# Kernel tuning notes

Measured on AMD Instinct MI355X. Metric: run time of the kernel, lower is better.

## Reference

```python
import jax, jax.numpy as jnp
import numpy as np
import math

B, HQ, HK, M, N, D, S, O, SO = 4, 32, 8, 16, 8192, 128, 256, 8, 64


def _make_proj_score(key):
    # __init__: randn proj, then per-D-column-chunk QR (rot=True), scaled by sqrt(D)
    proj = jax.random.normal(key, (D, S), dtype=jnp.float32)
    chunks = []
    for i in range(0, S, D):
        q, _ = jnp.linalg.qr(proj[:, i:i + D])
        chunks.append(q)
    return (jnp.concatenate(chunks, axis=-1) * math.sqrt(D)).astype(jnp.float32)


def setup_inputs() -> dict:
    key = jax.random.key(0)
    k1, k2, k3, k4 = jax.random.split(key, 4)
    return {
        "query": jax.random.normal(k1, (B, HQ, M, D), dtype=jnp.float32),
        "data": jax.random.normal(k2, (B, HK, N, D), dtype=jnp.float32),
        "proj_dir_score": _make_proj_score(k3),
        "outlier_indices": jax.random.randint(k4, (B, HK, N, O), 0, D, dtype=jnp.int32),
        "dim_outlier": SO,
    }


def reference(query, data, proj_dir_score, outlier_indices, dim_outlier):
    # query: [B,Hq,M,D] fp32; data (keys): [B,Hk,N,D]; proj_dir_score: [D,S]
    Bb, Hk, Nn, Dd = data.shape
    Hq, Mq = query.shape[1], query.shape[2]
    G = Hq // Hk  # GQA repeat factor (repeat_interleave along heads)
    Ss = proj_dir_score.shape[1]
    So = dim_outlier
    dt = data.dtype

    # --- qjl_quant: split keys into inlier / outlier channels per key ---
    # scatter a 0/1 outlier-channel mask: [B,Hk,N,D]
    flat_idx = outlier_indices.reshape(-1, outlier_indices.shape[-1])
    rows = jnp.arange(flat_idx.shape[0])[:, None]
    mask = jnp.zeros((flat_idx.shape[0], Dd), dt).at[rows, flat_idx].set(1.0)
    mask = mask.reshape(Bb, Hk, Nn, Dd)

    k_out = data * mask          # outlier channels only
    k_in = data - k_out          # outlier channels zeroed
    norm_in = jnp.linalg.norm(k_in, axis=-1)    # [B,Hk,N]
    norm_out = jnp.linalg.norm(k_out, axis=-1)  # [B,Hk,N]

    # 1-bit sign-JL quantization (bit-packed in the CUDA kernel; +-1 floats here)
    sign_in = jnp.sign(jnp.einsum('bhnd,ds->bhns', k_in, proj_dir_score))   # [B,Hk,N,S]
    proj_out = proj_dir_score[:, :So]                                       # [D,So]
    sign_out = jnp.sign(jnp.einsum('bhnd,ds->bhns', k_out, proj_out))       # [B,Hk,N,So]

    # --- qjl_gqa_score: QJL unbiased inner-product estimator ---
    # <q,k> ~= sqrt(pi/2)/m * ||k|| * <S q, sign(S k)>, inlier + outlier parts
    coef_in = math.sqrt(math.pi / 2.0) / Ss
    coef_out = math.sqrt(math.pi / 2.0) / So

    k_eff = sign_in * (coef_in * norm_in)[..., None]                        # [B,Hk,N,S]
    # fold outlier part back onto head-dim channels: w_eff[n,d] = mask * (sign_out @ proj_out^T)
    w_eff = mask * jnp.einsum('bhns,ds->bhnd', sign_out, proj_out)
    w_eff = w_eff * (coef_out * norm_out)[..., None]                        # [B,Hk,N,D]

    sketched_q = jnp.einsum('bhmd,ds->bhms', query, proj_dir_score)         # [B,Hq,M,S]
    # group query heads per kv head instead of repeat_interleaving keys (same math)
    sq_g = sketched_q.reshape(Bb, Hk, G, Mq, Ss)
    q_g = query.reshape(Bb, Hk, G, Mq, Dd)

    scores = (jnp.einsum('bhgms,bhns->bhgmn', sq_g, k_eff)
              + jnp.einsum('bhgmd,bhnd->bhgmn', q_g, w_eff))                # [B,Hk,G,M,N]
    scores = scores.reshape(Bb, Hq, Mq, Nn)
    return jnp.swapaxes(scores, -1, -2)  # final .transpose(-1,-2): [B,Hq,N,M]
```

## Files before the change

kernel.cpp:

```cpp
#include <hip/hip_runtime.h>
#include <hip/hip_bf16.h>
#include <math.h>

namespace {
constexpr int B_ = 4, HQ_ = 32, HK_ = 8, G_ = 4, M_ = 16;
constexpr int N_ = 8192, D_ = 128, S_ = 256, O_ = 8;
constexpr int TN = 64;
constexpr float TAU = 1e-3f;
}

typedef short short8 __attribute__((ext_vector_type(8)));
typedef float f32x4 __attribute__((ext_vector_type(4)));
typedef unsigned int uint4_ __attribute__((ext_vector_type(4)));

__device__ inline unsigned short f2bf_rne(float f) {
    unsigned u = __float_as_uint(f);
    u += 0x7FFF + ((u >> 16) & 1);
    return (unsigned short)(u >> 16);
}
__device__ inline float bf2f(unsigned short h) {
    return __uint_as_float(((unsigned)h) << 16);
}

__global__ __launch_bounds__(256) void qjl_prept(const float* __restrict__ P,
                                                 unsigned short* __restrict__ PtHi,
                                                 unsigned short* __restrict__ PtLo,
                                                 float* __restrict__ Pt32) {
    const int d = blockIdx.x;
    const int s = threadIdx.x;
    const float f = P[d * S_ + s];
    const unsigned short hb = f2bf_rne(f);
    const float lof = f - bf2f(hb);
    PtHi[s * D_ + d] = hb;
    PtLo[s * D_ + d] = f2bf_rne(lof);
    Pt32[s * D_ + d] = f;
}

__global__ __launch_bounds__(256) void qjl_sketch_q(const float* __restrict__ q,
                                                    const float* __restrict__ P,
                                                    unsigned short* __restrict__ sqHi) {
    __shared__ float qs[M_][D_];
    const int tid = threadIdx.x;
    const size_t blk = blockIdx.x;
    const float* qb = q + blk * (size_t)(M_ * D_);
    for (int i = tid; i < M_ * D_ / 4; i += 256)
        reinterpret_cast<float4*>(&qs[0][0])[i] = reinterpret_cast<const float4*>(qb)[i];
    __syncthreads();
    float acc[M_];
#pragma unroll
    for (int m = 0; m < M_; ++m) acc[m] = 0.f;
    const int s = tid;
    for (int d = 0; d < D_; ++d) {
        const float pv = P[d * S_ + s];
#pragma unroll
        for (int m = 0; m < M_; ++m) acc[m] = fmaf(qs[m][d], pv, acc[m]);
    }
    unsigned short* ob = sqHi + blk * (size_t)(M_ * S_);
#pragma unroll
    for (int m = 0; m < M_; ++m) ob[m * S_ + s] = f2bf_rne(acc[m]);
}

__device__ __noinline__ float qjl_fix_coop(const float* __restrict__ drow,
                                           const float* __restrict__ Pt32,
                                           int col, unsigned long long ip,
                                           float a, int src) {
    const int lane = threadIdx.x & 63;
    const float2 dv = *reinterpret_cast<const float2*>(&drow[2 * lane]);
    const float2 pv = *reinterpret_cast<const float2*>(&Pt32[(size_t)col * D_ + 2 * lane]);
    double p = 0.0;
#pragma unroll
    for (int e = 0; e < 2; ++e) {
        const int d = 2 * lane + e;
        const float v = e ? dv.y : dv.x;
        const float pw = e ? pv.y : pv.x;
        bool isout = false;
#pragma unroll
        for (int j = 0; j < 8; ++j)
            isout = isout || (((unsigned)(ip >> (8 * j)) & 0xFFu) == (unsigned)d);
        if (!isout) p = fma((double)v, (double)pw, p);
    }
#pragma unroll
    for (int off = 1; off < 64; off <<= 1) p += __shfl_xor(p, off);
    if (lane == src) a = (p > 0.0) ? 1.f : -1.f;
    return a;
}

__global__ __launch_bounds__(256) void qjl_main(const float* __restrict__ data,
                                                const float* __restrict__ q,
                                                const float* __restrict__ P,
                                                const int* __restrict__ oidx,
                                                const unsigned short* __restrict__ sqHi,
                                                const unsigned short* __restrict__ PtHi,
                                                const unsigned short* __restrict__ PtLo,
                                                const float* __restrict__ Pt32,
                                                float* __restrict__ out) {
    __shared__ unsigned short abuf[16384];
    __shared__ unsigned long long words[4][16][4];
    __shared__ float su2[TN][O_];
    __shared__ unsigned long long sidxp[TN];
    __shared__ float sfull[TN];
    __shared__ float snin[TN];
    __shared__ float snout[TN];

    const int tid = threadIdx.x;
    const int lane = tid & 63;
    const int wv = tid >> 6;
    const int l15 = lane & 15;
    const int kgrp = (lane >> 4) << 3;
    const int nt = blockIdx.x, hk = blockIdx.y, b = blockIdx.z;
    const int n0 = nt * TN;
    const float* dbase = data + ((size_t)(b * HK_ + hk) * N_) * D_;

    {
        const int r = tid >> 2;
        const int c = tid & 3;
        const float* drow = dbase + (size_t)(n0 + r) * D_;
        const int swz = (r & 7) << 3;
        float ssq = 0.f;
#pragma unroll
        for (int k = 0; k < 8; ++k) {
            const int f = c + 4 * k;
            float4 v = reinterpret_cast<const float4*>(drow)[f];
            ssq += v.x * v.x + v.y * v.y + v.z * v.z + v.w * v.w;
            unsigned short h0 = f2bf_rne(v.x), h1 = f2bf_rne(v.y),
                           h2 = f2bf_rne(v.z), h3 = f2bf_rne(v.w);
            unsigned short l0 = f2bf_rne(v.x - bf2f(h0)), l1 = f2bf_rne(v.y - bf2f(h1)),
                           l2 = f2bf_rne(v.z - bf2f(h2)), l3 = f2bf_rne(v.w - bf2f(h3));
            const int ei = r * 128 + ((4 * f) ^ swz);
            unsigned long long hw = (unsigned long long)h0 | ((unsigned long long)h1 << 16) |
                                    ((unsigned long long)h2 << 32) | ((unsigned long long)h3 << 48);
            unsigned long long lw = (unsigned long long)l0 | ((unsigned long long)l1 << 16) |
                                    ((unsigned long long)l2 << 32) | ((unsigned long long)l3 << 48);
            *reinterpret_cast<unsigned long long*>(&abuf[ei]) = hw;
            *reinterpret_cast<unsigned long long*>(&abuf[8192 + ei]) = lw;
        }
        ssq += __shfl_xor(ssq, 1);
        ssq += __shfl_xor(ssq, 2);
        if (c == 0) sfull[r] = ssq;
    }
    __syncthreads();

    if (tid < TN) {
        const int n = tid;
        const int* ob = oidx + ((size_t)(b * HK_ + hk) * N_ + n0 + n) * O_;
        const float* drow = dbase + (size_t)(n0 + n) * D_;
        int id[O_];
        int4 i0 = reinterpret_cast<const int4*>(ob)[0];
        int4 i1 = reinterpret_cast<const int4*>(ob)[1];
        id[0] = i0.x; id[1] = i0.y; id[2] = i0.z; id[3] = i0.w;
        id[4] = i1.x; id[5] = i1.y; id[6] = i1.z; id[7] = i1.w;
        const int swz = (n & 7) << 3;
        unsigned long long ip = 0;
        float so2 = 0.f;
#pragma unroll
        for (int j = 0; j < O_; ++j) {
            bool dup = false;
#pragma unroll
            for (int jj = 0; jj < O_; ++jj)
                if (jj < j) dup = dup || (id[jj] == id[j]);
            if (!dup) {
                const float v = drow[id[j]];
                so2 = fmaf(v, v, so2);
                ip |= (unsigned long long)(id[j] & 0xFF) << (8 * j);
                const int ei = n * 128 + (id[j] ^ swz);
                abuf[ei] = 0;
                abuf[8192 + ei] = 0;
            } else {
                ip |= 0xFFull << (8 * j);
            }
        }
        sidxp[n] = ip;
        const float CIN = (float)(1.2533141373155003 / 256.0);
        const float COUT = (float)(1.2533141373155003 / 64.0);
        snin[n] = CIN * sqrtf(fmaxf(sfull[n] - so2, 0.f));
        snout[n] = COUT * sqrtf(so2);
    }
    __syncthreads();

    {
        const int n = tid >> 2;
        const int c = tid & 3;
        const unsigned long long ip = sidxp[n];
        const float* drow = dbase + (size_t)(n0 + n) * D_;
        float u[O_], vv[O_];
        const float* pr[O_];
        bool val[O_];
#pragma unroll
        for (int j = 0; j < O_; ++j) {
            u[j] = 0.f;
            const unsigned bt = (unsigned)(ip >> (8 * j)) & 0xFFu;
            val[j] = (bt != 0xFFu);
            const int ix = (int)(bt & 0x7Fu);
            pr[j] = P + ix * S_;
            vv[j] = val[j] ? drow[ix] : 0.f;
        }
#pragma unroll
        for (int ch = 0; ch < 4; ++ch) {
            const int tc = c * 16 + ch * 4;
            float4 pj[O_];
#pragma unroll
            for (int j = 0; j < O_; ++j)
                pj[j] = *reinterpret_cast<const float4*>(pr[j] + tc);
#pragma unroll
            for (int e = 0; e < 4; ++e) {
                double cs = 0.0;
#pragma unroll
                for (int j = 0; j < O_; ++j)
                    cs = fma((double)vv[j], (double)pj[j][e], cs);
                const float sg = (cs > 0.0) ? 1.f : ((cs < 0.0) ? -1.f : 0.f);
#pragma unroll
                for (int j = 0; j < O_; ++j)
                    u[j] = fmaf(sg, pj[j][e], u[j]);
            }
        }
#pragma unroll
        for (int j = 0; j < O_; ++j) {
            u[j] += __shfl_xor(u[j], 1);
            u[j] += __shfl_xor(u[j], 2);
        }
        if (c == 0) {
            const float cno = snout[n];
#pragma unroll
            for (int j = 0; j < O_; ++j) su2[n][j] = val[j] ? u[j] * cno : 0.f;
        }
    }

    {
        const int t0 = wv * 4;
#pragma unroll
        for (int ti = 0; ti < 4; ++ti) {
            const int t = t0 + ti;
            short8 bhi[4], blo[4];
            const size_t bo = (size_t)(16 * t + l15) * D_ + kgrp;
#pragma unroll
            for (int ks = 0; ks < 4; ++ks) {
                bhi[ks] = *reinterpret_cast<const short8*>(PtHi + bo + ks * 32);
                blo[ks] = *reinterpret_cast<const short8*>(PtLo + bo + ks * 32);
            }
#pragma unroll
            for (int rt = 0; rt < 4; ++rt) {
                const int arow = 16 * rt + l15;
                const int aswz = (arow & 7) << 3;
                short8 ahi[4], alo[4];
#pragma unroll
                for (int ks = 0; ks < 4; ++ks) {
                    const int ei = arow * 128 + ((ks * 32 + kgrp) ^ aswz);
                    ahi[ks] = *reinterpret_cast<const short8*>(&abuf[ei]);
                    alo[ks] = *reinterpret_cast<const short8*>(&abuf[8192 + ei]);
                }
                f32x4 ac1 = (f32x4){0.f, 0.f, 0.f, 0.f};
                f32x4 ac2 = (f32x4){0.f, 0.f, 0.f, 0.f};
                f32x4 ac3 = (f32x4){0.f, 0.f, 0.f, 0.f};
#pragma unroll
                for (int ks = 0; ks < 4; ++ks) {
                    ac1 = __builtin_amdgcn_mfma_f32_16x16x32_bf16(ahi[ks], bhi[ks], ac1, 0, 0, 0);
                    ac2 = __builtin_amdgcn_mfma_f32_16x16x32_bf16(ahi[ks], blo[ks], ac2, 0, 0, 0);
                    ac3 = __builtin_amdgcn_mfma_f32_16x16x32_bf16(alo[ks], bhi[ks], ac3, 0, 0, 0);
                }
                f32x4 a = (ac1 + ac2) + ac3;
                const float mn = fminf(fminf(fabsf(a[0]), fabsf(a[1])),
                                       fminf(fabsf(a[2]), fabsf(a[3])));
                if (__ballot(mn < TAU) != 0ull) {
#pragma unroll
                    for (int r = 0; r < 4; ++r) {
                        unsigned long long low = __ballot(fabsf(a[r]) < TAU);
                        while (low) {
                            const int src = __ffsll((unsigned long long)low) - 1;
                            low &= low - 1;
                            const int row = 16 * rt + ((src >> 4) << 2) + r;
                            const int col = 16 * t + (src & 15);
                            a[r] = qjl_fix_coop(dbase + (size_t)(n0 + row) * D_, Pt32, col,
                                                sidxp[row], a[r], src);
                        }
                    }
                }
#pragma unroll
                for (int r = 0; r < 4; ++r) {
                    const unsigned long long bb = __ballot(a[r] > 0.f);
                    if (lane == 0) words[rt][t][r] = bb;
                }
            }
        }
    }

    const int hq = hk * G_ + wv;
    const unsigned short* sqb = sqHi + (size_t)(b * HQ_ + hq) * (M_ * S_);
    short8 aq[8];
#pragma unroll
    for (int ks = 0; ks < 8; ++ks)
        aq[ks] = *reinterpret_cast<const short8*>(sqb + (size_t)l15 * S_ + ks * 32 + kgrp);
    __syncthreads();

    {
        const int n = tid & 63;
        const int c64 = tid >> 6;
        const unsigned short cb = f2bf_rne(snin[n]);
        const unsigned base = (unsigned)cb | ((unsigned)cb << 16);
        const int g = (n >> 2) & 3;
        const int r = n & 3;
        const int w = n >> 4;
        const int swz = (n & 7) << 3;
#pragma unroll
        for (int i = 0; i < 4; ++i) {
            const int t = c64 * 4 + i;
            const unsigned long long wd = words[w][t][r];
            const unsigned bits = (unsigned)(wd >> (16 * g)) & 0xFFFFu;
            const unsigned nb = ~bits;
            unsigned o[8];
#pragma unroll
            for (int p = 0; p < 8; ++p) {
                const unsigned m = (((nb >> (2 * p)) & 1u) << 15) |
                                   (((nb >> (2 * p + 1)) & 1u) << 31);
                o[p] = base ^ m;
            }
            const int s0 = c64 * 64 + i * 16;
            const int e0 = n * 256 + (s0 ^ swz);
            const int e1 = n * 256 + ((s0 + 8) ^ swz);
            *reinterpret_cast<uint4_*>(&abuf[e0]) = (uint4_){o[0], o[1], o[2], o[3]};
            *reinterpret_cast<uint4_*>(&abuf[e1]) = (uint4_){o[4], o[5], o[6], o[7]};
        }
    }
    __syncthreads();

    {
        const float* qhead = q + (size_t)(b * HQ_ + hq) * (M_ * D_);
        const int m0 = (lane >> 4) << 2;
#pragma unroll
        for (int ct = 0; ct < 4; ++ct) {
            const int n = 16 * ct + l15;
            const int nswz = (n & 7) << 3;
            f32x4 acc = (f32x4){0.f, 0.f, 0.f, 0.f};
#pragma unroll
            for (int ks = 0; ks < 8; ++ks) {
                const int ei = n * 256 + ((ks * 32 + kgrp) ^ nswz);
                const short8 bs = *reinterpret_cast<const short8*>(&abuf[ei]);
                acc = __builtin_amdgcn_mfma_f32_16x16x32_bf16(aq[ks], bs, acc, 0, 0, 0);
            }
            const f32x4 s01 = *reinterpret_cast<const f32x4*>(&su2[n][0]);
            const f32x4 s23 = *reinterpret_cast<const f32x4*>(&su2[n][4]);
            const unsigned long long ip = sidxp[n];
            float a0 = 0.f, a1 = 0.f, a2 = 0.f, a3 = 0.f;
#pragma unroll
            for (int j = 0; j < O_; ++j) {
                const float uj = (j < 4) ? s01[j & 3] : s23[j & 3];
                const int ix = (int)((ip >> (8 * j)) & 0x7Fu);
                const float* qp = qhead + ix;
                a0 = fmaf(uj, qp[(m0 + 0) * D_], a0);
                a1 = fmaf(uj, qp[(m0 + 1) * D_], a1);
                a2 = fmaf(uj, qp[(m0 + 2) * D_], a2);
                a3 = fmaf(uj, qp[(m0 + 3) * D_], a3);
            }
            acc[0] += a0; acc[1] += a1; acc[2] += a2; acc[3] += a3;
            float* ob = out + ((size_t)(b * HQ_ + hq) * N_ + (n0 + n)) * M_ + m0;
            *reinterpret_cast<f32x4*>(ob) = acc;
        }
    }
}

extern "C" void kernel_launch(void* const* d_in, const int* in_sizes, int n_in,
                              void* d_out, int out_size, void* d_ws, size_t ws_size,
                              hipStream_t stream) {
    const float* query = (const float*)d_in[0];
    const float* data  = (const float*)d_in[1];
    const float* proj  = (const float*)d_in[2];
    const int*   oidx  = (const int*)d_in[3];

    float* out = (float*)d_out;
    unsigned short* sqHi = (unsigned short*)d_ws;
    unsigned short* PtHi = (unsigned short*)((char*)d_ws + (1 << 20));
    unsigned short* PtLo = (unsigned short*)((char*)d_ws + (1 << 20) + (64 << 10));
    float*          Pt32 = (float*)((char*)d_ws + (1 << 20) + (128 << 10));

    qjl_prept<<<dim3(D_), dim3(S_), 0, stream>>>(proj, PtHi, PtLo, Pt32);
    qjl_sketch_q<<<dim3(B_ * HQ_), dim3(256), 0, stream>>>(query, proj, sqHi);
    qjl_main<<<dim3(N_ / TN, HK_, B_), dim3(256), 0, stream>>>(data, query, proj, oidx,
                                                               sqHi, PtHi, PtLo, Pt32, out);
}
```

Measured before the change: 250.9 us.

## Split main kernel into sign-computation and output kernels via global intermediates

Splits the fused main kernel into two kernels. One computes the sign words, norms, outlier weights and indices and writes them to workspace; the other builds the bf16 sign matrix and runs the MFMA scores. The split is meant to cut per-kernel LDS and register pressure so occupancy rises, at the cost of an extra launch and a global round-trip of intermediates. The change also adds a transposed query copy so outlier query loads can be float4 vectors, and replaces the double-precision outlier sign projection with float plus a double fallback near zero.

```diff
diff --git a/kernel.cpp b/kernel.cpp
--- a/kernel.cpp
+++ b/kernel.cpp
@@ -6,12 +6,14 @@
 constexpr int B_ = 4, HQ_ = 32, HK_ = 8, G_ = 4, M_ = 16;
 constexpr int N_ = 8192, D_ = 128, S_ = 256, O_ = 8;
 constexpr int TN = 64;
-constexpr float TAU = 1e-3f;
+constexpr float TAU  = 1e-3f;
+constexpr float TAUO = 1e-4f;
 }
 
 typedef short short8 __attribute__((ext_vector_type(8)));
 typedef float f32x4 __attribute__((ext_vector_type(4)));
 typedef unsigned int uint4_ __attribute__((ext_vector_type(4)));
+typedef unsigned long long ull2 __attribute__((ext_vector_type(2)));
 
 __device__ inline unsigned short f2bf_rne(float f) {
     unsigned u = __float_as_uint(f);
@@ -38,7 +40,8 @@
 
 __global__ __launch_bounds__(256) void qjl_sketch_q(const float* __restrict__ q,
                                                     const float* __restrict__ P,
-                                                    unsigned short* __restrict__ sqHi) {
+                                                    unsigned short* __restrict__ sqHi,
+                                                    float* __restrict__ qT) {
     __shared__ float qs[M_][D_];
     const int tid = threadIdx.x;
     const size_t blk = blockIdx.x;
@@ -46,6 +49,17 @@
     for (int i = tid; i < M_ * D_ / 4; i += 256)
         reinterpret_cast<float4*>(&qs[0][0])[i] = reinterpret_cast<const float4*>(qb)[i];
     __syncthreads();
+    float* qtb = qT + blk * (size_t)(D_ * M_);
+    for (int i = tid; i < D_ * M_ / 4; i += 256) {
+        const int d = i >> 2;
+        const int m4 = i & 3;
+        float4 v;
+        v.x = qs[m4 * 4 + 0][d];
+        v.y = qs[m4 * 4 + 1][d];
+        v.z = qs[m4 * 4 + 2][d];
+        v.w = qs[m4 * 4 + 3][d];
+        reinterpret_cast<float4*>(qtb)[i] = v;
+    }
     float acc[M_];
 #pragma unroll
     for (int m = 0; m < M_; ++m) acc[m] = 0.f;
@@ -85,21 +99,19 @@
     return a;
 }
 
-__global__ __launch_bounds__(256) void qjl_main(const float* __restrict__ data,
-                                                const float* __restrict__ q,
-                                                const float* __restrict__ P,
-                                                const int* __restrict__ oidx,
-                                                const unsigned short* __restrict__ sqHi,
-                                                const unsigned short* __restrict__ PtHi,
-                                                const unsigned short* __restrict__ PtLo,
-                                                const float* __restrict__ Pt32,
-                                                float* __restrict__ out) {
+__global__ __launch_bounds__(256) void qjl_signs(const float* __restrict__ data,
+                                                 const float* __restrict__ P,
+                                                 const int* __restrict__ oidx,
+                                                 const unsigned short* __restrict__ PtHi,
+                                                 const unsigned short* __restrict__ PtLo,
+                                                 const float* __restrict__ Pt32,
+                                                 unsigned long long* __restrict__ wordsg,
+                                                 float* __restrict__ sning,
+                                                 float* __restrict__ su2g,
+                                                 unsigned long long* __restrict__ sidxpg) {
     __shared__ unsigned short abuf[16384];
-    __shared__ unsigned long long words[4][16][4];
-    __shared__ float su2[TN][O_];
     __shared__ unsigned long long sidxp[TN];
     __shared__ float sfull[TN];
-    __shared__ float snin[TN];
     __shared__ float snout[TN];
 
     const int tid = threadIdx.x;
@@ -109,6 +121,8 @@
     const int kgrp = (lane >> 4) << 3;
     const int nt = blockIdx.x, hk = blockIdx.y, b = blockIdx.z;
     const int n0 = nt * TN;
+    const size_t rowbase = (size_t)(b * HK_ + hk) * N_ + n0;
+    const size_t wblk = (size_t)((b * HK_ + hk) * (N_ / TN) + nt);
     const float* dbase = data + ((size_t)(b * HK_ + hk) * N_) * D_;
 
     {
@@ -170,9 +184,10 @@
             }
         }
         sidxp[n] = ip;
+        sidxpg[rowbase + n] = ip;
         const float CIN = (float)(1.2533141373155003 / 256.0);
         const float COUT = (float)(1.2533141373155003 / 64.0);
-        snin[n] = CIN * sqrtf(fmaxf(sfull[n] - so2, 0.f));
+        sning[rowbase + n] = CIN * sqrtf(fmaxf(sfull[n] - so2, 0.f));
         snout[n] = COUT * sqrtf(so2);
     }
     __syncthreads();
@@ -203,11 +218,20 @@
                 pj[j] = *reinterpret_cast<const float4*>(pr[j] + tc);
 #pragma unroll
             for (int e = 0; e < 4; ++e) {
-                double cs = 0.0;
+                float cs = 0.f;
 #pragma unroll
                 for (int j = 0; j < O_; ++j)
-                    cs = fma((double)vv[j], (double)pj[j][e], cs);
-                const float sg = (cs > 0.0) ? 1.f : ((cs < 0.0) ? -1.f : 0.f);
+                    cs = fmaf(vv[j], pj[j][e], cs);
+                float sg;
+                if (fabsf(cs) < TAUO) {
+                    double cd = 0.0;
+#pragma unroll
+                    for (int j = 0; j < O_; ++j)
+                        cd = fma((double)vv[j], (double)pj[j][e], cd);
+                    sg = (cd > 0.0) ? 1.f : ((cd < 0.0) ? -1.f : 0.f);
+                } else {
+                    sg = (cs > 0.f) ? 1.f : -1.f;
+                }
 #pragma unroll
                 for (int j = 0; j < O_; ++j)
                     u[j] = fmaf(sg, pj[j][e], u[j]);
@@ -220,8 +244,12 @@
         }
         if (c == 0) {
             const float cno = snout[n];
-#pragma unroll
-            for (int j = 0; j < O_; ++j) su2[n][j] = val[j] ? u[j] * cno : 0.f;
+            float o[O_];
+#pragma unroll
+            for (int j = 0; j < O_; ++j) o[j] = val[j] ? u[j] * cno : 0.f;
+            float* sp = su2g + (rowbase + n) * O_;
+            *reinterpret_cast<f32x4*>(sp) = (f32x4){o[0], o[1], o[2], o[3]};
+            *reinterpret_cast<f32x4*>(sp + 4) = (f32x4){o[4], o[5], o[6], o[7]};
         }
     }
 
@@ -274,36 +302,60 @@
                         }
                     }
                 }
-#pragma unroll
-                for (int r = 0; r < 4; ++r) {
-                    const unsigned long long bb = __ballot(a[r] > 0.f);
-                    if (lane == 0) words[rt][t][r] = bb;
+                unsigned long long bb0 = __ballot(a[0] > 0.f);
+                unsigned long long bb1 = __ballot(a[1] > 0.f);
+                unsigned long long bb2 = __ballot(a[2] > 0.f);
+                unsigned long long bb3 = __ballot(a[3] > 0.f);
+                if (lane == 0) {
+                    unsigned long long* wp = wordsg + (wblk * 256 + (size_t)(rt * 16 + t) * 4);
+                    *reinterpret_cast<ull2*>(wp) = (ull2){bb0, bb1};
+                    *reinterpret_cast<ull2*>(wp + 2) = (ull2){bb2, bb3};
                 }
             }
         }
     }
-
+}
+
+__global__ __launch_bounds__(256) void qjl_out(const unsigned short* __restrict__ sqHi,
+                                               const float* __restrict__ qT,
+                                               const unsigned long long* __restrict__ wordsg,
+                                               const float* __restrict__ sning,
+                                               const float* __restrict__ su2g,
+                                               const unsigned long long* __restrict__ sidxpg,
+                                               float* __restrict__ out) {
+    __shared__ unsigned short scol[16384];
+
+    const int tid = threadIdx.x;
+    const int lane = tid & 63;
+    const int wv = tid >> 6;
+    const int l15 = lane & 15;
+    const int kgrp = (lane >> 4) << 3;
+    const int nt = blockIdx.x, hk = blockIdx.y, b = blockIdx.z;
+    const int n0 = nt * TN;
+    const size_t rowbase = (size_t)(b * HK_ + hk) * N_ + n0;
+    const size_t wblk = (size_t)((b * HK_ + hk) * (N_ / TN) + nt);
     const int hq = hk * G_ + wv;
+
     const unsigned short* sqb = sqHi + (size_t)(b * HQ_ + hq) * (M_ * S_);
     short8 aq[8];
 #pragma unroll
     for (int ks = 0; ks < 8; ++ks)
         aq[ks] = *reinterpret_cast<const short8*>(sqb + (size_t)l15 * S_ + ks * 32 + kgrp);
-    __syncthreads();
 
     {
         const int n = tid & 63;
         const int c64 = tid >> 6;
-        const unsigned short cb = f2bf_rne(snin[n]);
+        const unsigned short cb = f2bf_rne(sning[rowbase + n]);
         const unsigned base = (unsigned)cb | ((unsigned)cb << 16);
         const int g = (n >> 2) & 3;
         const int r = n & 3;
         const int w = n >> 4;
         const int swz = (n & 7) << 3;
+        const unsigned long long* wbp = wordsg + wblk * 256;
 #pragma unroll
         for (int i = 0; i < 4; ++i) {
             const int t = c64 * 4 + i;
-            const unsigned long long wd = words[w][t][r];
+            const unsigned long long wd = wbp[(size_t)(w * 16 + t) * 4 + r];
             const unsigned bits = (unsigned)(wd >> (16 * g)) & 0xFFFFu;
             const unsigned nb = ~bits;
             unsigned o[8];
@@ -316,39 +368,40 @@
             const int s0 = c64 * 64 + i * 16;
             const int e0 = n * 256 + (s0 ^ swz);
             const int e1 = n * 256 + ((s0 + 8) ^ swz);
-            *reinterpret_cast<uint4_*>(&abuf[e0]) = (uint4_){o[0], o[1], o[2], o[3]};
-            *reinterpret_cast<uint4_*>(&abuf[e1]) = (uint4_){o[4], o[5], o[6], o[7]};
+            *reinterpret_cast<uint4_*>(&scol[e0]) = (uint4_){o[0], o[1], o[2], o[3]};
+            *reinterpret_cast<uint4_*>(&scol[e1]) = (uint4_){o[4], o[5], o[6], o[7]};
         }
     }
     __syncthreads();
 
     {
-        const float* qhead = q + (size_t)(b * HQ_ + hq) * (M_ * D_);
+        const float* qtb = qT + (size_t)(b * HQ_ + hq) * (D_ * M_);
         const int m0 = (lane >> 4) << 2;
 #pragma unroll
         for (int ct = 0; ct < 4; ++ct) {
             const int n = 16 * ct + l15;
+            const size_t row = rowbase + n;
+            const unsigned long long ip = sidxpg[row];
+            const f32x4 s01 = *reinterpret_cast<const f32x4*>(su2g + row * O_);
+            const f32x4 s23 = *reinterpret_cast<const f32x4*>(su2g + row * O_ + 4);
             const int nswz = (n & 7) << 3;
             f32x4 acc = (f32x4){0.f, 0.f, 0.f, 0.f};
 #pragma unroll
             for (int ks = 0; ks < 8; ++ks) {
                 const int ei = n * 256 + ((ks * 32 + kgrp) ^ nswz);
-                const short8 bs = *reinterpret_cast<const short8*>(&abuf[ei]);
+                const short8 bs = *reinterpret_cast<const short8*>(&scol[ei]);
                 acc = __builtin_amdgcn_mfma_f32_16x16x32_bf16(aq[ks], bs, acc, 0, 0, 0);
             }
-            const f32x4 s01 = *reinterpret_cast<const f32x4*>(&su2[n][0]);
-            const f32x4 s23 = *reinterpret_cast<const f32x4*>(&su2[n][4]);
-            const unsigned long long ip = sidxp[n];
             float a0 = 0.f, a1 = 0.f, a2 = 0.f, a3 = 0.f;
 #pragma unroll
             for (int j = 0; j < O_; ++j) {
                 const float uj = (j < 4) ? s01[j & 3] : s23[j & 3];
                 const int ix = (int)((ip >> (8 * j)) & 0x7Fu);
-                const float* qp = qhead + ix;
-                a0 = fmaf(uj, qp[(m0 + 0) * D_], a0);
-                a1 = fmaf(uj, qp[(m0 + 1) * D_], a1);
-                a2 = fmaf(uj, qp[(m0 + 2) * D_], a2);
-                a3 = fmaf(uj, qp[(m0 + 3) * D_], a3);
+                const float4 qv = *reinterpret_cast<const float4*>(qtb + ix * M_ + m0);
+                a0 = fmaf(uj, qv.x, a0);
+                a1 = fmaf(uj, qv.y, a1);
+                a2 = fmaf(uj, qv.z, a2);
+                a3 = fmaf(uj, qv.w, a3);
             }
             acc[0] += a0; acc[1] += a1; acc[2] += a2; acc[3] += a3;
             float* ob = out + ((size_t)(b * HQ_ + hq) * N_ + (n0 + n)) * M_ + m0;
@@ -366,13 +419,22 @@
     const int*   oidx  = (const int*)d_in[3];
 
     float* out = (float*)d_out;
-    unsigned short* sqHi = (unsigned short*)d_ws;
-    unsigned short* PtHi = (unsigned short*)((char*)d_ws + (1 << 20));
-    unsigned short* PtLo = (unsigned short*)((char*)d_ws + (1 << 20) + (64 << 10));
-    float*          Pt32 = (float*)((char*)d_ws + (1 << 20) + (128 << 10));
+
+    char* ws = (char*)d_ws;
+    unsigned short* sqHi  = (unsigned short*)(ws);
+    float*          qT    = (float*)(ws + (1 << 20));
+    unsigned short* PtHi  = (unsigned short*)(ws + (2 << 20));
+    unsigned short* PtLo  = (unsigned short*)(ws + (2 << 20) + (64 << 10));
+    float*          Pt32  = (float*)(ws + (2 << 20) + (128 << 10));
+    unsigned long long* wordsg = (unsigned long long*)(ws + (3 << 20));
+    float*          sning = (float*)(ws + (11 << 20));
+    float*          su2g  = (float*)(ws + (12 << 20));
+    unsigned long long* sidxpg = (unsigned long long*)(ws + (20 << 20));
 
     qjl_prept<<<dim3(D_), dim3(S_), 0, stream>>>(proj, PtHi, PtLo, Pt32);
-    qjl_sketch_q<<<dim3(B_ * HQ_), dim3(256), 0, stream>>>(query, proj, sqHi);
-    qjl_main<<<dim3(N_ / TN, HK_, B_), dim3(256), 0, stream>>>(data, query, proj, oidx,
-                                                               sqHi, PtHi, PtLo, Pt32, out);
-}
+    qjl_sketch_q<<<dim3(B_ * HQ_), dim3(256), 0, stream>>>(query, proj, sqHi, qT);
+    qjl_signs<<<dim3(N_ / TN, HK_, B_), dim3(256), 0, stream>>>(
+        data, proj, oidx, PtHi, PtLo, Pt32, wordsg, sning, su2g, sidxpg);
+    qjl_out<<<dim3(N_ / TN, HK_, B_), dim3(256), 0, stream>>>(
+        sqHi, qT, wordsg, sning, su2g, sidxpg, out);
+}
```

After: 215.0 us. -14.3%, faster.
